# Optimization experiments

Hardware: AMD Instinct MI355X
Metric: run time of the kernel (lower is better)

The kernel has to match this reference:

```python
import jax, jax.numpy as jnp
import numpy as np

B, L, D = 1, 4096, 2048
H, KVH, HD = 8, 2, 256
WINDOW = 512
BASE = 10000.0
ROPE_FRACTION = 1.0


def _rms_norm(x, scale=None):
    x32 = x.astype(jnp.float32)
    var = jnp.mean(jnp.square(x32), axis=-1, keepdims=True)
    xn = x32 * jax.lax.rsqrt(var + 1e-6)
    return xn if scale is None else xn * scale.astype(jnp.float32)


def _apply_rope(x, positions, base, rope_fraction):
    head_dim = x.shape[-1]
    rope_dim = int(head_dim * rope_fraction)
    if rope_dim == 0:
        return x
    half = rope_dim // 2
    head_half = head_dim // 2
    freq_exp = 2.0 * jnp.arange(half, dtype=jnp.float32) / head_dim
    timescale = base ** freq_exp
    pos = positions[..., None].astype(jnp.float32)          # [B, L, 1]
    sinusoid = pos / timescale[None, None, :]               # [B, L, half]
    sin = jnp.sin(sinusoid)[:, :, None, :]                  # [B, L, 1, half]
    cos = jnp.cos(sinusoid)[:, :, None, :]
    x1 = x[..., :half]
    x2 = x[..., head_half:head_half + half]
    x1r = x1 * cos - x2 * sin
    x2r = x2 * cos + x1 * sin
    if rope_dim == head_dim:
        return jnp.concatenate([x1r, x2r], axis=-1)
    return jnp.concatenate(
        [x1r, x[..., half:head_half], x2r, x[..., head_half + half:]], axis=-1)


def setup_inputs() -> dict:
    key = jax.random.key(0)
    ks = jax.random.split(key, 5)
    x = jax.random.normal(ks[0], (B, L, D), dtype=jnp.float32)
    positions = jnp.broadcast_to(jnp.arange(L, dtype=jnp.int32)[None, :], (B, L))
    s = 0.02
    Wq = jax.random.normal(ks[1], (D, H * HD), dtype=jnp.float32) * s
    Wk = jax.random.normal(ks[2], (D, KVH * HD), dtype=jnp.float32) * s
    Wv = jax.random.normal(ks[3], (D, KVH * HD), dtype=jnp.float32) * s
    Wo = jax.random.normal(ks[4], (H * HD, D), dtype=jnp.float32) * s
    q_scale = jnp.ones((HD,), dtype=jnp.float32)
    k_scale = jnp.ones((HD,), dtype=jnp.float32)
    return {"x": x, "positions": positions, "Wq": Wq, "Wk": Wk, "Wv": Wv,
            "Wo": Wo, "q_scale": q_scale, "k_scale": k_scale}


def reference(x, positions, Wq, Wk, Wv, Wo, q_scale, k_scale):
    # projections (no bias, no 1/sqrt(d) scaling, matching the source)
    q = (x @ Wq).reshape(B, L, H, HD)
    k = (x @ Wk).reshape(B, L, KVH, HD)
    v = (x @ Wv).reshape(B, L, KVH, HD)
    # QK RMSNorm (learned scale), V RMSNorm (no scale)
    q = _apply_rope(_rms_norm(q, q_scale), positions, BASE, ROPE_FRACTION)
    k = _apply_rope(_rms_norm(k, k_scale), positions, BASE, ROPE_FRACTION)
    v = _rms_norm(v)
    # GQA head repeat
    rep = H // KVH
    k = jnp.repeat(k, rep, axis=2)  # [B, L, H, HD]
    v = jnp.repeat(v, rep, axis=2)
    # attention scores [B, H, Lq, Lk]
    scores = jnp.einsum('bqhd,bkhd->bhqk', q, k)
    qi = jnp.arange(L)[:, None]
    kj = jnp.arange(L)[None, :]
    mask = (kj <= qi) & (kj >= qi - WINDOW + 1)  # causal & sliding window
    scores = jnp.where(mask[None, None, :, :], scores, -10000.0)
    probs = jax.nn.softmax(scores.astype(jnp.float32), axis=-1)
    out = jnp.einsum('bhqk,bkhd->bqhd', probs, v)
    return out.reshape(B, L, H * HD) @ Wo
```

## Files before the change

kernel.cpp:

```cpp
#include <hip/hip_runtime.h>
#include <hip/hip_bf16.h>
#include <math.h>
#include <stdint.h>

#define L_      4096
#define D_      2048
#define H_      8
#define KVH_    2
#define HD_     256
#define WINDOW_ 512
#define QKVW    3072

typedef __attribute__((ext_vector_type(8))) _Float16 f16x8;
typedef __attribute__((ext_vector_type(4))) _Float16 f16x4;
typedef __attribute__((ext_vector_type(4))) short s16x4;
typedef __attribute__((ext_vector_type(4))) float f32x4;

__device__ __forceinline__ short f2h(float f) {
    _Float16 h = (_Float16)f;
    return *reinterpret_cast<short*>(&h);
}
__device__ __forceinline__ float h2f(short s) {
    _Float16 h = *reinterpret_cast<_Float16*>(&s);
    return (float)h;
}

__device__ __forceinline__ void gl2lds16(const void* g, void* l) {
    __builtin_amdgcn_global_load_lds(
        (const __attribute__((address_space(1))) uint32_t*)g,
        (__attribute__((address_space(3))) uint32_t*)l, 16, 0, 0);
}

__global__ __launch_bounds__(256) void cast_f16(const float* __restrict__ X,
                                                short* __restrict__ Y, int n) {
    int idx = (blockIdx.x * 256 + threadIdx.x) * 8;
    if (idx >= n) return;
    float4 a = *(const float4*)(X + idx);
    float4 b = *(const float4*)(X + idx + 4);
    s16x4 o0, o1;
    o0[0]=f2h(a.x); o0[1]=f2h(a.y); o0[2]=f2h(a.z); o0[3]=f2h(a.w);
    o1[0]=f2h(b.x); o1[1]=f2h(b.y); o1[2]=f2h(b.z); o1[3]=f2h(b.w);
    *(s16x4*)(Y + idx)     = o0;
    *(s16x4*)(Y + idx + 4) = o1;
}

__global__ __launch_bounds__(256) void transpose_cast(const float* __restrict__ W,
                                                      short* __restrict__ Wt,
                                                      int K, int N) {
    __shared__ float tl[32][33];
    int t = threadIdx.x;
    int c = t & 31, r4 = (t >> 5) * 4;
    int k0 = blockIdx.y * 32, n0 = blockIdx.x * 32;
#pragma unroll
    for (int i = 0; i < 4; ++i)
        tl[r4 + i][c] = W[(size_t)(k0 + r4 + i) * N + n0 + c];
    __syncthreads();
#pragma unroll
    for (int i = 0; i < 4; ++i)
        Wt[(size_t)(n0 + r4 + i) * K + k0 + c] = f2h(tl[c][r4 + i]);
}

template <int OUT_HALF>
__global__ __launch_bounds__(256) void gemm_mfma(const short* __restrict__ A,
                                                 const short* __restrict__ Bt,
                                                 void* __restrict__ Cout,
                                                 int M, int N, int K) {
    __shared__ short As[128][64];
    __shared__ short Bs[128][64];

    const int tid = threadIdx.x;
    const int w = tid >> 6, lane = tid & 63;
    const int lq = lane & 15, quad = lane >> 4;
    const int bm = blockIdx.y * 128, bn = blockIdx.x * 128;
    const int wm = (w & 1) * 64, wn = (w >> 1) * 64;
    const int lrow = lane >> 3;
    const int slot = lane & 7;

    f32x4 acc[4][4];
#pragma unroll
    for (int i = 0; i < 4; ++i)
#pragma unroll
        for (int j = 0; j < 4; ++j) acc[i][j] = 0;

    for (int k0 = 0; k0 < K; k0 += 64) {
#pragma unroll
        for (int c = 0; c < 4; ++c) {
            const int r0 = w * 32 + c * 8;
            const int row = r0 + lrow;
            const int chunk = slot ^ (row & 7);
            gl2lds16(A  + (size_t)(bm + row) * K + k0 + chunk * 8, &As[r0][0]);
            gl2lds16(Bt + (size_t)(bn + row) * K + k0 + chunk * 8, &Bs[r0][0]);
        }
        __syncthreads();

#pragma unroll
        for (int f = 0; f < 2; ++f) {
            const int sA = (((f * 4) + quad) ^ (lq & 7)) * 8;
            f16x8 af[4], bfr[4];
#pragma unroll
            for (int i = 0; i < 4; ++i) af[i]  = *(const f16x8*)&As[wm + i * 16 + lq][sA];
#pragma unroll
            for (int j = 0; j < 4; ++j) bfr[j] = *(const f16x8*)&Bs[wn + j * 16 + lq][sA];
#pragma unroll
            for (int i = 0; i < 4; ++i)
#pragma unroll
                for (int j = 0; j < 4; ++j)
                    acc[i][j] = __builtin_amdgcn_mfma_f32_16x16x32_f16(af[i], bfr[j], acc[i][j], 0, 0, 0);
        }
        __syncthreads();
    }

#pragma unroll
    for (int i = 0; i < 4; ++i)
#pragma unroll
        for (int r = 0; r < 4; ++r) {
            int row = bm + wm + i * 16 + quad * 4 + r;
#pragma unroll
            for (int j = 0; j < 4; ++j) {
                int col = bn + wn + j * 16 + lq;
                float v = acc[i][j][r];
                if (OUT_HALF) ((short*)Cout)[(size_t)row * N + col] = f2h(v);
                else          ((float*)Cout)[(size_t)row * N + col] = v;
            }
        }
}

__global__ __launch_bounds__(256) void norm_rope_w(short* __restrict__ qkv,
                                                   const float* __restrict__ q_scale,
                                                   const float* __restrict__ k_scale,
                                                   const int* __restrict__ positions) {
    const int w = threadIdx.x >> 6, lane = threadIdx.x & 63;
    const int row = blockIdx.x * 4 + w;
    const int token = row / 12, ridx = row % 12;
    short* p = qkv + (size_t)token * QKVW + ridx * HD_ + lane * 4;

    const s16x4 raw = *(const s16x4*)p;
    float xv[4];
#pragma unroll
    for (int i = 0; i < 4; ++i) xv[i] = h2f(raw[i]);
    float ss = xv[0]*xv[0] + xv[1]*xv[1] + xv[2]*xv[2] + xv[3]*xv[3];
#pragma unroll
    for (int off = 32; off > 0; off >>= 1) ss += __shfl_xor(ss, off);
    const float rinv = rsqrtf(ss * (1.0f / (float)HD_) + 1e-6f);
#pragma unroll
    for (int i = 0; i < 4; ++i) xv[i] *= rinv;

    if (ridx < 10) {
        const float* scp = (ridx < 8 ? q_scale : k_scale) + lane * 4;
        const float4 sc = *(const float4*)scp;
        xv[0] *= sc.x; xv[1] *= sc.y; xv[2] *= sc.z; xv[3] *= sc.w;

        const int pos = positions[token];
        float ov[4];
#pragma unroll
        for (int i = 0; i < 4; ++i) ov[i] = __shfl_xor(xv[i], 32);
        const float sgn = (lane < 32) ? -1.0f : 1.0f;
        const int dbase = (lane & 31) * 4;
#pragma unroll
        for (int i = 0; i < 4; ++i) {
            const float fe = (float)(dbase + i) * (1.0f / 128.0f);
            const float inv_ts = __expf(fe * -9.210340371976184f);
            const float ang = (float)pos * inv_ts;
            float s, c;
            __sincosf(ang, &s, &c);
            xv[i] = xv[i] * c + sgn * ov[i] * s;
        }
    }

    s16x4 o;
#pragma unroll
    for (int i = 0; i < 4; ++i) o[i] = f2h(xv[i]);
    *(s16x4*)p = o;
}

__global__ __launch_bounds__(256) void vt_prep(const short* __restrict__ qkv,
                                               short* __restrict__ vtg) {
    const int tok0 = blockIdx.x * 64;
    const int g = blockIdx.y;
    const int tid = threadIdx.x;
    __shared__ short Vs[64][264];
#pragma unroll
    for (int i = 0; i < 8; ++i) {
        int f = (tid + i * 256) * 8;
        int tok = f >> 8, d = f & 255;
        *(int4*)&Vs[tok][d] =
            *(const int4*)(qkv + (size_t)(tok0 + tok) * QKVW + 2560 + g * HD_ + d);
    }
    __syncthreads();
    const int d = tid;
    short tmp[64];
#pragma unroll
    for (int j = 0; j < 64; ++j) tmp[j] = Vs[j][d];
    short* dst = vtg + ((size_t)g * HD_ + d) * L_ + tok0;
#pragma unroll
    for (int c = 0; c < 8; ++c)
        *(int4*)(dst + c * 8) = *(const int4*)&tmp[c * 8];
}

__global__ __launch_bounds__(256) void attn_mfma(const short* __restrict__ qkv,
                                                 const short* __restrict__ vtg,
                                                 short* __restrict__ ao) {
    const int bx = blockIdx.x;
    const int g = bx & 1, qt = bx >> 1;
    const int q0 = qt * 16;
    const int tid = threadIdx.x;
    const int w = tid >> 6, lane = tid & 63;
    const int lq = lane & 15, quad = lane >> 4;
    const int h = g * 4 + w;

    __shared__ short lds[32768];

    f16x8 qf[8];
    {
        const short* qrow = qkv + (size_t)(q0 + lq) * QKVW + h * HD_;
#pragma unroll
        for (int f = 0; f < 8; ++f)
            qf[f] = *(const f16x8*)(qrow + f * 32 + quad * 8);
    }

    float m_run = -INFINITY, l_run = 0.0f;

    f32x4 accO[16];
#pragma unroll
    for (int dt = 0; dt < 16; ++dt) accO[dt] = 0;

    const short* kcol = qkv + 2048 + g * HD_;
    const short* vrow = vtg + (size_t)g * HD_ * L_;
    const int qi = q0 + lq;

    const int kl5 = lane >> 5;
    const int ksl = lane & 31;
    const int vdm = ((lane >> 5) << 3) | (lane & 7);
    const int vkc = (lane >> 3) & 3;

    auto stageKV = [&](int b, int kb) {
#pragma unroll
        for (int i = 0; i < 4; ++i) {
            const int r0 = w * 8 + 2 * i;
            const int row = r0 + kl5;
            const int cs = ksl ^ (row & 7);
            const int kj = min(max(kb + row, 0), L_ - 1);
            gl2lds16(kcol + (size_t)kj * QKVW + cs * 8, lds + b * 8192 + r0 * 256);
        }
        const int ck = min(max(kb + vkc * 8, 0), L_ - 8);
#pragma unroll
        for (int j = 0; j < 4; ++j) {
            const int wv = w * 4 + j;
            gl2lds16(vrow + (size_t)(wv * 16 + vdm) * L_ + ck,
                     lds + 16384 + b * 8192 + wv * 512);
        }
    };

    const int kt0 = (q0 >= 480) ? 0 : ((480 - q0) / 32 + 1);
    int buf = 0;
    stageKV(0, q0 - WINDOW_ + kt0 * 32);

    for (int kt = kt0; kt < 17; ++kt) {
        const int kbase = q0 - WINDOW_ + kt * 32;
        if (kt < 16) {
            stageKV(buf ^ 1, kbase + 32);
            asm volatile("s_waitcnt vmcnt(8)" ::: "memory");
        } else {
            asm volatile("s_waitcnt vmcnt(0)" ::: "memory");
        }
        __builtin_amdgcn_s_barrier();
        __builtin_amdgcn_sched_barrier(0);

        const short* KsB = lds + buf * 8192;
        const short* VtB = lds + 16384 + buf * 8192;

        f32x4 st0 = 0, st1 = 0;
        __builtin_amdgcn_s_setprio(1);
#pragma unroll
        for (int f = 0; f < 8; ++f) {
            const int sl = ((f * 4 + quad) ^ (lq & 7)) * 8;
            f16x8 kf0 = *(const f16x8*)(KsB + lq * 256 + sl);
            f16x8 kf1 = *(const f16x8*)(KsB + (16 + lq) * 256 + sl);
            st0 = __builtin_amdgcn_mfma_f32_16x16x32_f16(kf0, qf[f], st0, 0, 0, 0);
            st1 = __builtin_amdgcn_mfma_f32_16x16x32_f16(kf1, qf[f], st1, 0, 0, 0);
        }
        __builtin_amdgcn_s_setprio(0);

        const int kA = kbase + quad * 4;
        const int kB = kA + 16;
        float sv[8]; bool vd[8];
#pragma unroll
        for (int r = 0; r < 4; ++r) {
            int ka = kA + r, kb2 = kB + r;
            vd[r]     = (ka >= 0) && (ka <= qi) && (ka > qi - WINDOW_);
            vd[4 + r] = (kb2 >= 0) && (kb2 <= qi) && (kb2 > qi - WINDOW_);
            sv[r]     = vd[r]     ? st0[r] : -INFINITY;
            sv[4 + r] = vd[4 + r] ? st1[r] : -INFINITY;
        }
        float mt = sv[0];
#pragma unroll
        for (int i = 1; i < 8; ++i) mt = fmaxf(mt, sv[i]);
        mt = fmaxf(mt, __shfl_xor(mt, 16));
        mt = fmaxf(mt, __shfl_xor(mt, 32));
        const float mn = fmaxf(m_run, mt);
        const float alpha = (mn == -INFINITY) ? 1.0f : __expf(m_run - mn);
        float pv[8], rs = 0.0f;
#pragma unroll
        for (int i = 0; i < 8; ++i) {
            pv[i] = vd[i] ? __expf(sv[i] - mn) : 0.0f;
            rs += pv[i];
        }
        rs += __shfl_xor(rs, 16);
        rs += __shfl_xor(rs, 32);
        m_run = mn;
        l_run = l_run * alpha + rs;

        f16x4 p0, p1;
#pragma unroll
        for (int i = 0; i < 4; ++i) { p0[i] = (_Float16)pv[i]; p1[i] = (_Float16)pv[4 + i]; }

        const int sl0 = ((lq >> 3) << 5) | ((quad >> 1) << 3) | (lq & 7);
        const int hh = (quad & 1) * 4;
        __builtin_amdgcn_s_setprio(1);
#pragma unroll
        for (int dt = 0; dt < 16; ++dt) {
            f16x4 v0 = *(const f16x4*)(VtB + dt * 512 + sl0 * 8 + hh);
            f16x4 v1 = *(const f16x4*)(VtB + dt * 512 + (sl0 | 16) * 8 + hh);
            f32x4 t = accO[dt];
#pragma unroll
            for (int r = 0; r < 4; ++r) t[r] *= alpha;
            t = __builtin_amdgcn_mfma_f32_16x16x16f16(v0, p0, t, 0, 0, 0);
            t = __builtin_amdgcn_mfma_f32_16x16x16f16(v1, p1, t, 0, 0, 0);
            accO[dt] = t;
        }
        __builtin_amdgcn_s_setprio(0);

        __builtin_amdgcn_s_barrier();
        __builtin_amdgcn_sched_barrier(0);
        buf ^= 1;
    }

    const float inv = 1.0f / l_run;
    short* myE = lds + w * 4224;
#pragma unroll
    for (int dt = 0; dt < 16; ++dt) {
        f16x4 e;
#pragma unroll
        for (int r = 0; r < 4; ++r) e[r] = (_Float16)(accO[dt][r] * inv);
        *(f16x4*)&myE[lq * 264 + dt * 16 + quad * 4] = e;
    }
    {
        const int row = lane >> 2;
        const int c0 = (lane & 3) * 64;
        short* orow = ao + (size_t)(q0 + row) * 2048 + h * HD_ + c0;
#pragma unroll
        for (int u = 0; u < 8; ++u)
            *(int4*)(orow + u * 8) = *(const int4*)&myE[row * 264 + c0 + u * 8];
    }
}

extern "C" void kernel_launch(void* const* d_in, const int* in_sizes, int n_in,
                              void* d_out, int out_size, void* d_ws, size_t ws_size,
                              hipStream_t stream) {
    const float* x         = (const float*)d_in[0];
    const int*   positions = (const int*)d_in[1];
    const float* Wq        = (const float*)d_in[2];
    const float* Wk        = (const float*)d_in[3];
    const float* Wv        = (const float*)d_in[4];
    const float* Wo        = (const float*)d_in[5];
    const float* q_scale   = (const float*)d_in[6];
    const float* k_scale   = (const float*)d_in[7];
    float*       out       = (float*)d_out;

    char* ws = (char*)d_ws;
    short* xb    = (short*)(ws);
    short* qkv   = (short*)(ws + 16777216);
    short* ao    = (short*)(ws + 41943040);
    short* Wtqkv = (short*)(ws + 58720256);
    short* Wto   = (short*)(ws + 71303168);
    short* vtg   = xb;

    cast_f16<<<4096, 256, 0, stream>>>(x, xb, L_ * D_);
    transpose_cast<<<dim3(2048 / 32, 2048 / 32), 256, 0, stream>>>(Wq, Wtqkv, D_, 2048);
    transpose_cast<<<dim3(512 / 32, 2048 / 32), 256, 0, stream>>>(Wk, Wtqkv + (size_t)2048 * D_, D_, 512);
    transpose_cast<<<dim3(512 / 32, 2048 / 32), 256, 0, stream>>>(Wv, Wtqkv + (size_t)2560 * D_, D_, 512);
    transpose_cast<<<dim3(2048 / 32, 2048 / 32), 256, 0, stream>>>(Wo, Wto, 2048, 2048);

    gemm_mfma<1><<<dim3(QKVW / 128, L_ / 128), 256, 0, stream>>>(xb, Wtqkv, qkv, L_, QKVW, D_);

    norm_rope_w<<<(L_ * 12) / 4, 256, 0, stream>>>(qkv, q_scale, k_scale, positions);

    vt_prep<<<dim3(L_ / 64, KVH_), 256, 0, stream>>>(qkv, vtg);

    attn_mfma<<<(L_ / 16) * KVH_, 256, 0, stream>>>(qkv, vtg, ao);

    gemm_mfma<0><<<dim3(D_ / 128, L_ / 128), 256, 0, stream>>>(ao, Wto, out, L_, D_, 2048);
}
```

Measured before the change: 301.0 us.

## Use 256x256 tiled double-buffered MFMA GEMM for QKV projection

Adds a new GEMM kernel with 256x256 block tiles, 512 threads, double-buffered LDS staging through direct global-to-LDS loads, XOR-swizzled LDS layout, quarter-phase interleaving of loads and MFMAs, and a workgroup index swizzle. It replaces the 128x128 GEMM for the QKV projection to raise arithmetic intensity and overlap memory with compute. The trade-off is a large LDS footprint (128KB) and high register use, which limits occupancy. The grid is also small (12x16 blocks), which may leave compute units underused.

Result: slower. 309.0 us (+2.7%).

```diff
diff --git a/kernel.cpp b/kernel.cpp
--- a/kernel.cpp
+++ b/kernel.cpp
@@ -119,6 +119,129 @@
             for (int j = 0; j < 4; ++j) {
                 int col = bn + wn + j * 16 + lq;
                 float v = acc[i][j][r];
+                if (OUT_HALF) ((short*)Cout)[(size_t)row * N + col] = f2h(v);
+                else          ((float*)Cout)[(size_t)row * N + col] = v;
+            }
+        }
+}
+
+template <int OUT_HALF>
+__global__ __launch_bounds__(512, 2) void gemm_mfma256(const short* __restrict__ A,
+                                                       const short* __restrict__ Bt,
+                                                       void* __restrict__ Cout,
+                                                       int M, int N, int K) {
+    __shared__ short As[2][256][64];
+    __shared__ short Bs[2][256][64];
+
+    const int tid = threadIdx.x;
+    const int w = tid >> 6, lane = tid & 63;
+    const int lq = lane & 15, quad = lane >> 4;
+    const int lq7 = lq & 7;
+    const int wm128 = (w >> 2) * 128;
+    const int wn = (w & 3) * 64;
+
+    int bid = blockIdx.y * gridDim.x + blockIdx.x;
+    int nwg = gridDim.x * gridDim.y;
+    int qch = nwg >> 3;
+    int swz = (bid & 7) * qch + (bid >> 3);
+    const int bn = (swz % gridDim.x) * 256;
+    const int bm = (swz / gridDim.x) * 256;
+
+    const int KT = K >> 6, KTm1 = KT - 1;
+
+    auto stageA = [&](int s, int kt2, int mq) {
+        const int k0 = min(kt2, KTm1) * 64;
+#pragma unroll
+        for (int i = 0; i < 2; ++i) {
+            const int r0 = i * 128 + mq * 64 + w * 8;
+            const int row = r0 + (lane >> 3);
+            const int chunk = (lane & 7) ^ (row & 7);
+            gl2lds16(A + (size_t)(bm + row) * K + k0 + chunk * 8, &As[s][r0][0]);
+        }
+    };
+    auto stageB = [&](int s, int kt2, int nq) {
+        const int k0 = min(kt2, KTm1) * 64;
+#pragma unroll
+        for (int i = 0; i < 2; ++i) {
+            const int g = i * 2 + (w >> 2);
+            const int r0 = g * 64 + nq * 32 + (w & 3) * 8;
+            const int row = r0 + (lane >> 3);
+            const int chunk = (lane & 7) ^ (row & 7);
+            gl2lds16(Bt + (size_t)(bn + row) * K + k0 + chunk * 8, &Bs[s][r0][0]);
+        }
+    };
+
+    f32x4 acc[8][4];
+#pragma unroll
+    for (int i = 0; i < 8; ++i)
+#pragma unroll
+        for (int j = 0; j < 4; ++j) acc[i][j] = 0;
+
+    f16x8 af[4][2];
+    f16x8 bf[2][2][2];
+
+#define QPHASE(S, MQ, NQ, READA, READB, STAGE_STMT)                              \
+    do {                                                                         \
+        if (READA) {                                                             \
+            _Pragma("unroll") for (int i_ = 0; i_ < 4; ++i_)                     \
+            _Pragma("unroll") for (int ks_ = 0; ks_ < 2; ++ks_)                  \
+                af[i_][ks_] = *(const f16x8*)&As[S][wm128 + (MQ)*64 + i_*16 + lq]\
+                                                   [((ks_*4 + quad) ^ lq7) * 8]; \
+        }                                                                        \
+        if (READB) {                                                             \
+            _Pragma("unroll") for (int j_ = 0; j_ < 2; ++j_)                     \
+            _Pragma("unroll") for (int ks_ = 0; ks_ < 2; ++ks_)                  \
+                bf[NQ][j_][ks_] = *(const f16x8*)&Bs[S][wn + (NQ)*32 + j_*16 + lq]\
+                                                     [((ks_*4 + quad) ^ lq7) * 8]; \
+        }                                                                        \
+        STAGE_STMT;                                                              \
+        asm volatile("s_waitcnt vmcnt(6)" ::: "memory");                         \
+        __builtin_amdgcn_s_barrier();                                            \
+        asm volatile("s_waitcnt lgkmcnt(0)" ::: "memory");                       \
+        __builtin_amdgcn_sched_barrier(0);                                       \
+        __builtin_amdgcn_s_setprio(1);                                           \
+        _Pragma("unroll") for (int i_ = 0; i_ < 4; ++i_)                         \
+        _Pragma("unroll") for (int j_ = 0; j_ < 2; ++j_) {                       \
+            acc[(MQ)*4 + i_][(NQ)*2 + j_] = __builtin_amdgcn_mfma_f32_16x16x32_f16( \
+                af[i_][0], bf[NQ][j_][0], acc[(MQ)*4 + i_][(NQ)*2 + j_], 0, 0, 0);  \
+            acc[(MQ)*4 + i_][(NQ)*2 + j_] = __builtin_amdgcn_mfma_f32_16x16x32_f16( \
+                af[i_][1], bf[NQ][j_][1], acc[(MQ)*4 + i_][(NQ)*2 + j_], 0, 0, 0);  \
+        }                                                                        \
+        __builtin_amdgcn_s_setprio(0);                                           \
+        __builtin_amdgcn_s_barrier();                                            \
+    } while (0)
+
+    stageA(0, 0, 0);
+    stageB(0, 0, 0);
+    stageB(0, 0, 1);
+    stageA(0, 0, 1);
+    stageA(1, 1, 0);
+    asm volatile("s_waitcnt vmcnt(6)" ::: "memory");
+    __builtin_amdgcn_s_barrier();
+
+    for (int kt = 0; kt < KT; kt += 2) {
+        QPHASE(0, 0, 0, 1, 1, stageB(1, kt + 1, 0));
+        QPHASE(0, 0, 1, 0, 1, stageB(1, kt + 1, 1));
+        QPHASE(0, 1, 0, 1, 0, stageA(1, kt + 1, 1));
+        QPHASE(0, 1, 1, 0, 0, stageA(0, kt + 2, 0));
+        QPHASE(1, 0, 0, 1, 1, stageB(0, kt + 2, 0));
+        QPHASE(1, 0, 1, 0, 1, stageB(0, kt + 2, 1));
+        QPHASE(1, 1, 0, 1, 0, stageA(0, kt + 2, 1));
+        QPHASE(1, 1, 1, 0, 0, stageA(1, kt + 3, 0));
+    }
+#undef QPHASE
+
+    asm volatile("s_waitcnt vmcnt(0)" ::: "memory");
+
+#pragma unroll
+    for (int mi = 0; mi < 8; ++mi)
+#pragma unroll
+        for (int r = 0; r < 4; ++r) {
+            int row = bm + wm128 + mi * 16 + quad * 4 + r;
+#pragma unroll
+            for (int j = 0; j < 4; ++j) {
+                int col = bn + wn + j * 16 + lq;
+                float v = acc[mi][j][r];
                 if (OUT_HALF) ((short*)Cout)[(size_t)row * N + col] = f2h(v);
                 else          ((float*)Cout)[(size_t)row * N + col] = v;
             }
@@ -381,7 +504,7 @@
     transpose_cast<<<dim3(512 / 32, 2048 / 32), 256, 0, stream>>>(Wv, Wtqkv + (size_t)2560 * D_, D_, 512);
     transpose_cast<<<dim3(2048 / 32, 2048 / 32), 256, 0, stream>>>(Wo, Wto, 2048, 2048);
 
-    gemm_mfma<1><<<dim3(QKVW / 128, L_ / 128), 256, 0, stream>>>(xb, Wtqkv, qkv, L_, QKVW, D_);
+    gemm_mfma256<1><<<dim3(QKVW / 256, L_ / 256), 512, 0, stream>>>(xb, Wtqkv, qkv, L_, QKVW, D_);
 
     norm_rope_w<<<(L_ * 12) / 4, 256, 0, stream>>>(qkv, q_scale, k_scale, positions);
 
```

## Fuse prep kernels, fold V norm into transpose, add lazy softmax rescale

Applied to the files above, without the earlier changes.

Merges the input cast and the four weight transpose-casts into one launch. Merges Q/K norm+RoPE with the V transpose, computing V's RMS norm inside the transpose block so the separate V norm pass goes away. In attention, the running-max rescale of the output accumulator is skipped unless some row's tile max exceeds the running max by more than 8. This removes per-iteration alpha multiplies at the cost of a wave-uniform branch and a small risk of fp16 overflow in the probabilities.

Result: no change. 295.8 us (-1.7%).

```diff
diff --git a/kernel.cpp b/kernel.cpp
--- a/kernel.cpp
+++ b/kernel.cpp
@@ -31,26 +31,39 @@
         (__attribute__((address_space(3))) uint32_t*)l, 16, 0, 0);
 }
 
-__global__ __launch_bounds__(256) void cast_f16(const float* __restrict__ X,
-                                                short* __restrict__ Y, int n) {
-    int idx = (blockIdx.x * 256 + threadIdx.x) * 8;
-    if (idx >= n) return;
-    float4 a = *(const float4*)(X + idx);
-    float4 b = *(const float4*)(X + idx + 4);
-    s16x4 o0, o1;
-    o0[0]=f2h(a.x); o0[1]=f2h(a.y); o0[2]=f2h(a.z); o0[3]=f2h(a.w);
-    o1[0]=f2h(b.x); o1[1]=f2h(b.y); o1[2]=f2h(b.z); o1[3]=f2h(b.w);
-    *(s16x4*)(Y + idx)     = o0;
-    *(s16x4*)(Y + idx + 4) = o1;
-}
-
-__global__ __launch_bounds__(256) void transpose_cast(const float* __restrict__ W,
-                                                      short* __restrict__ Wt,
-                                                      int K, int N) {
+__global__ __launch_bounds__(256) void prep_fused(const float* __restrict__ x,
+                                                  short* __restrict__ xb,
+                                                  const float* __restrict__ Wq,
+                                                  const float* __restrict__ Wk,
+                                                  const float* __restrict__ Wv,
+                                                  const float* __restrict__ Wo,
+                                                  short* __restrict__ Wtqkv,
+                                                  short* __restrict__ Wto) {
     __shared__ float tl[32][33];
-    int t = threadIdx.x;
-    int c = t & 31, r4 = (t >> 5) * 4;
-    int k0 = blockIdx.y * 32, n0 = blockIdx.x * 32;
+    const int bid = blockIdx.x;
+    const int t = threadIdx.x;
+
+    if (bid < 4096) {
+        int idx = (bid * 256 + t) * 8;
+        float4 a = *(const float4*)(x + idx);
+        float4 b = *(const float4*)(x + idx + 4);
+        s16x4 o0, o1;
+        o0[0]=f2h(a.x); o0[1]=f2h(a.y); o0[2]=f2h(a.z); o0[3]=f2h(a.w);
+        o1[0]=f2h(b.x); o1[1]=f2h(b.y); o1[2]=f2h(b.z); o1[3]=f2h(b.w);
+        *(s16x4*)(xb + idx)     = o0;
+        *(s16x4*)(xb + idx + 4) = o1;
+        return;
+    }
+
+    const float* W; short* Wt; int N; int rb;
+    if (bid < 8192)       { W = Wq; Wt = Wtqkv;                       N = 2048; rb = bid - 4096; }
+    else if (bid < 9216)  { W = Wk; Wt = Wtqkv + (size_t)2048 * D_;   N = 512;  rb = bid - 8192; }
+    else if (bid < 10240) { W = Wv; Wt = Wtqkv + (size_t)2560 * D_;   N = 512;  rb = bid - 9216; }
+    else                  { W = Wo; Wt = Wto;                         N = 2048; rb = bid - 10240; }
+    const int K = 2048;
+    const int nb = N >> 5;
+    const int n0 = (rb % nb) * 32, k0 = (rb / nb) * 32;
+    const int c = t & 31, r4 = (t >> 5) * 4;
 #pragma unroll
     for (int i = 0; i < 4; ++i)
         tl[r4 + i][c] = W[(size_t)(k0 + r4 + i) * N + n0 + c];
@@ -125,30 +138,34 @@
         }
 }
 
-__global__ __launch_bounds__(256) void norm_rope_w(short* __restrict__ qkv,
-                                                   const float* __restrict__ q_scale,
-                                                   const float* __restrict__ k_scale,
-                                                   const int* __restrict__ positions) {
-    const int w = threadIdx.x >> 6, lane = threadIdx.x & 63;
-    const int row = blockIdx.x * 4 + w;
-    const int token = row / 12, ridx = row % 12;
-    short* p = qkv + (size_t)token * QKVW + ridx * HD_ + lane * 4;
-
-    const s16x4 raw = *(const s16x4*)p;
-    float xv[4];
-#pragma unroll
-    for (int i = 0; i < 4; ++i) xv[i] = h2f(raw[i]);
-    float ss = xv[0]*xv[0] + xv[1]*xv[1] + xv[2]*xv[2] + xv[3]*xv[3];
-#pragma unroll
-    for (int off = 32; off > 0; off >>= 1) ss += __shfl_xor(ss, off);
-    const float rinv = rsqrtf(ss * (1.0f / (float)HD_) + 1e-6f);
-#pragma unroll
-    for (int i = 0; i < 4; ++i) xv[i] *= rinv;
-
-    if (ridx < 10) {
+__global__ __launch_bounds__(256) void normvt_fused(short* __restrict__ qkv,
+                                                    const float* __restrict__ q_scale,
+                                                    const float* __restrict__ k_scale,
+                                                    const int* __restrict__ positions,
+                                                    short* __restrict__ vtg) {
+    __shared__ short Vs[64][264];
+    __shared__ float ri[64];
+    const int bid = blockIdx.x;
+    const int tid = threadIdx.x;
+
+    if (bid < 10240) {
+        const int w = tid >> 6, lane = tid & 63;
+        const int r = bid * 4 + w;
+        const int token = r / 10, ridx = r % 10;
+        short* p = qkv + (size_t)token * QKVW + ridx * HD_ + lane * 4;
+
+        const s16x4 raw = *(const s16x4*)p;
+        float xv[4];
+#pragma unroll
+        for (int i = 0; i < 4; ++i) xv[i] = h2f(raw[i]);
+        float ss = xv[0]*xv[0] + xv[1]*xv[1] + xv[2]*xv[2] + xv[3]*xv[3];
+#pragma unroll
+        for (int off = 32; off > 0; off >>= 1) ss += __shfl_xor(ss, off);
+        const float rinv = rsqrtf(ss * (1.0f / (float)HD_) + 1e-6f);
         const float* scp = (ridx < 8 ? q_scale : k_scale) + lane * 4;
         const float4 sc = *(const float4*)scp;
-        xv[0] *= sc.x; xv[1] *= sc.y; xv[2] *= sc.z; xv[3] *= sc.w;
+        xv[0] *= rinv * sc.x; xv[1] *= rinv * sc.y;
+        xv[2] *= rinv * sc.z; xv[3] *= rinv * sc.w;
 
         const int pos = positions[token];
         float ov[4];
@@ -165,20 +182,16 @@
             __sincosf(ang, &s, &c);
             xv[i] = xv[i] * c + sgn * ov[i] * s;
         }
-    }
-
-    s16x4 o;
-#pragma unroll
-    for (int i = 0; i < 4; ++i) o[i] = f2h(xv[i]);
-    *(s16x4*)p = o;
-}
-
-__global__ __launch_bounds__(256) void vt_prep(const short* __restrict__ qkv,
-                                               short* __restrict__ vtg) {
-    const int tok0 = blockIdx.x * 64;
-    const int g = blockIdx.y;
-    const int tid = threadIdx.x;
-    __shared__ short Vs[64][264];
+        s16x4 o;
+#pragma unroll
+        for (int i = 0; i < 4; ++i) o[i] = f2h(xv[i]);
+        *(s16x4*)p = o;
+        return;
+    }
+
+    const int rb = bid - 10240;
+    const int tok0 = (rb >> 1) * 64;
+    const int g = rb & 1;
 #pragma unroll
     for (int i = 0; i < 8; ++i) {
         int f = (tid + i * 256) * 8;
@@ -187,10 +200,24 @@
             *(const int4*)(qkv + (size_t)(tok0 + tok) * QKVW + 2560 + g * HD_ + d);
     }
     __syncthreads();
+    {
+        const int t = tid >> 2, s = tid & 3;
+        float ss = 0.0f;
+#pragma unroll
+        for (int d2 = 0; d2 < 16; ++d2) {
+            s16x4 v4 = *(const s16x4*)&Vs[t][s * 64 + d2 * 4];
+#pragma unroll
+            for (int k2 = 0; k2 < 4; ++k2) { float val = h2f(v4[k2]); ss += val * val; }
+        }
+        ss += __shfl_xor(ss, 1);
+        ss += __shfl_xor(ss, 2);
+        if (s == 0) ri[t] = rsqrtf(ss * (1.0f / (float)HD_) + 1e-6f);
+    }
+    __syncthreads();
     const int d = tid;
     short tmp[64];
 #pragma unroll
-    for (int j = 0; j < 64; ++j) tmp[j] = Vs[j][d];
+    for (int j = 0; j < 64; ++j) tmp[j] = f2h(h2f(Vs[j][d]) * ri[j]);
     short* dst = vtg + ((size_t)g * HD_ + d) * L_ + tok0;
 #pragma unroll
     for (int c = 0; c < 8; ++c)
@@ -297,18 +324,27 @@
         for (int i = 1; i < 8; ++i) mt = fmaxf(mt, sv[i]);
         mt = fmaxf(mt, __shfl_xor(mt, 16));
         mt = fmaxf(mt, __shfl_xor(mt, 32));
-        const float mn = fmaxf(m_run, mt);
-        const float alpha = (mn == -INFINITY) ? 1.0f : __expf(m_run - mn);
+
+        if (!__all(mt <= m_run + 8.0f)) {
+            const float mn = fmaxf(m_run, mt);
+            const float alpha = (mn == -INFINITY) ? 1.0f : __expf(m_run - mn);
+            m_run = mn;
+            l_run *= alpha;
+#pragma unroll
+            for (int dt = 0; dt < 16; ++dt)
+#pragma unroll
+                for (int r = 0; r < 4; ++r) accO[dt][r] *= alpha;
+        }
+
         float pv[8], rs = 0.0f;
 #pragma unroll
         for (int i = 0; i < 8; ++i) {
-            pv[i] = vd[i] ? __expf(sv[i] - mn) : 0.0f;
+            pv[i] = vd[i] ? __expf(sv[i] - m_run) : 0.0f;
             rs += pv[i];
         }
         rs += __shfl_xor(rs, 16);
         rs += __shfl_xor(rs, 32);
-        m_run = mn;
-        l_run = l_run * alpha + rs;
+        l_run += rs;
 
         f16x4 p0, p1;
 #pragma unroll
@@ -322,8 +358,6 @@
             f16x4 v0 = *(const f16x4*)(VtB + dt * 512 + sl0 * 8 + hh);
             f16x4 v1 = *(const f16x4*)(VtB + dt * 512 + (sl0 | 16) * 8 + hh);
             f32x4 t = accO[dt];
-#pragma unroll
-            for (int r = 0; r < 4; ++r) t[r] *= alpha;
             t = __builtin_amdgcn_mfma_f32_16x16x16f16(v0, p0, t, 0, 0, 0);
             t = __builtin_amdgcn_mfma_f32_16x16x16f16(v1, p1, t, 0, 0, 0);
             accO[dt] = t;
@@ -375,17 +409,11 @@
     short* Wto   = (short*)(ws + 71303168);
     short* vtg   = xb;
 
-    cast_f16<<<4096, 256, 0, stream>>>(x, xb, L_ * D_);
-    transpose_cast<<<dim3(2048 / 32, 2048 / 32), 256, 0, stream>>>(Wq, Wtqkv, D_, 2048);
-    transpose_cast<<<dim3(512 / 32, 2048 / 32), 256, 0, stream>>>(Wk, Wtqkv + (size_t)2048 * D_, D_, 512);
-    transpose_cast<<<dim3(512 / 32, 2048 / 32), 256, 0, stream>>>(Wv, Wtqkv + (size_t)2560 * D_, D_, 512);
-    transpose_cast<<<dim3(2048 / 32, 2048 / 32), 256, 0, stream>>>(Wo, Wto, 2048, 2048);
+    prep_fused<<<14336, 256, 0, stream>>>(x, xb, Wq, Wk, Wv, Wo, Wtqkv, Wto);
 
     gemm_mfma<1><<<dim3(QKVW / 128, L_ / 128), 256, 0, stream>>>(xb, Wtqkv, qkv, L_, QKVW, D_);
 
-    norm_rope_w<<<(L_ * 12) / 4, 256, 0, stream>>>(qkv, q_scale, k_scale, positions);
-
-    vt_prep<<<dim3(L_ / 64, KVH_), 256, 0, stream>>>(qkv, vtg);
+    normvt_fused<<<10368, 256, 0, stream>>>(qkv, q_scale, k_scale, positions, vtg);
 
     attn_mfma<<<(L_ / 16) * KVH_, 256, 0, stream>>>(qkv, vtg, ao);
 
```
